# Kernel optimization log

Measured on AMD Instinct MI355X. Metric: run time of the kernel, lower is better.

Reference implementation:

```python
import jax, jax.numpy as jnp
import numpy as np

N = 4096
CIN = 128
COUT = 128
J = 2
SLOPE = 0.2        # LeakyReLU negative slope (GAT-style)
NEG = -9.0e15      # mask fill value from the source
ATT = J * COUT     # att_slice


def _leaky(v):
    return jnp.where(v >= 0, v, SLOPE * v)


def setup_inputs() -> dict:
    key = jax.random.key(0)
    ks = jax.random.split(key, 12)
    x = jax.random.normal(ks[0], (N, CIN), dtype=jnp.float32)

    def sparse_op(k):
        kv, km = jax.random.split(k)
        vals = jax.random.normal(kv, (N, N), dtype=jnp.float32)
        mask = jax.random.uniform(km, (N, N)) < 0.05
        return jnp.where(mask, vals, 0.0)

    Lu = sparse_op(ks[1])
    Ld = sparse_op(ks[2])
    P = jax.random.normal(ks[3], (N, N), dtype=jnp.float32) * 0.01  # harmonic projector

    s = 1.0 / np.sqrt(CIN)
    Wi_w = jax.random.uniform(ks[4], (J, CIN, COUT), minval=-s, maxval=s)
    Wi_b = jax.random.uniform(ks[5], (J, COUT), minval=-s, maxval=s)
    Ws_w = jax.random.uniform(ks[6], (J, CIN, COUT), minval=-s, maxval=s)
    Ws_b = jax.random.uniform(ks[7], (J, COUT), minval=-s, maxval=s)
    Wh_w = jax.random.uniform(ks[8], (CIN, COUT), minval=-s, maxval=s)
    Wh_b = jax.random.uniform(ks[9], (COUT,), minval=-s, maxval=s)
    att_irr = jax.random.normal(ks[10], (2 * ATT, 1), dtype=jnp.float32) * 0.1
    att_sol = jax.random.normal(ks[11], (2 * ATT, 1), dtype=jnp.float32) * 0.1
    return {"x": x, "Lu": Lu, "Ld": Ld, "P": P,
            "Wi_w": Wi_w, "Wi_b": Wi_b, "Ws_w": Ws_w, "Ws_b": Ws_b,
            "Wh_w": Wh_w, "Wh_b": Wh_b, "att_irr": att_irr, "att_sol": att_sol}


def reference(x, Lu, Ld, P, Wi_w, Wi_b, Ws_w, Ws_b, Wh_w, Wh_b, att_irr, att_sol):
    n = x.shape[0]
    # concat_j W_irr[j](x) -> [N, J*COUT] (j-major matches torch.cat along dim=1)
    x_irr = (jnp.einsum('nc,jco->njo', x, Wi_w) + Wi_b[None]).reshape(n, ATT)
    x_sol = (jnp.einsum('nc,jco->njo', x, Ws_w) + Ws_b[None]).reshape(n, ATT)

    # GAT-style scores: E[i,j] = leaky(s1[i] + s2[j])
    E_irr = _leaky(x_irr @ att_irr[:ATT] + (x_irr @ att_irr[ATT:]).T)
    E_sol = _leaky(x_sol @ att_sol[:ATT] + (x_sol @ att_sol[ATT:]).T)
    E_irr = jnp.where(Ld != 0, E_irr, NEG)
    E_sol = jnp.where(Lu != 0, E_sol, NEG)
    alpha_irr = jax.nn.softmax(E_irr, axis=1)  # dropout: eval mode -> identity
    alpha_sol = jax.nn.softmax(E_sol, axis=1)

    z = (alpha_irr @ x) @ Wi_w[0] + Wi_b[0] + (alpha_sol @ x) @ Ws_w[0] + Ws_b[0]
    for p in range(1, J):  # Laplacian-power aggregation
        alpha_irr = alpha_irr @ Ld
        alpha_sol = alpha_sol @ Lu
        z = z + (alpha_irr @ x) @ Wi_w[p] + Wi_b[p]
        z = z + (alpha_sol @ x) @ Ws_w[p] + Ws_b[p]
    z = z + (P @ x) @ Wh_w + Wh_b
    return z
```

## Files before the change

kernel.cpp:

```cpp
#include <hip/hip_runtime.h>

#define NN 4096
#define IDX_CAP 512
#define SEG_CAP 160
#define SLOPE 0.2f

typedef float f4_t __attribute__((ext_vector_type(4)));

#define V_OFF     0
#define C_OFF     512
#define BT_OFF    516
#define S_OFF     1024
#define HXI_OFF   32768
#define HXS_OFF   (HXI_OFF + NN*128)
#define UI_OFF    (HXS_OFF + NN*128)
#define US_OFF    (UI_OFF + NN*128)
#define XWH_OFF   (US_OFF + NN*128)
#define OI_OFF    (XWH_OFF + NN*128)
#define OS_OFF    (OI_OFF + NN*128)
#define ZP_OFF    (OS_OFF + NN*128)
#define WS_FLOATS (ZP_OFF + 8*NN*128)
#define IDX_BYTE_OFF ((size_t)WS_FLOATS * 4)
#define CNT_BYTE_OFF (IDX_BYTE_OFF + (size_t)2*NN*IDX_CAP*2)

#define XI(c)   ((c) + (((c) >> 5) << 2))

#define MAP_BR(bid)   (((bid) >> 2) & 1)
#define MAP_ROW(bid)  ((((bid) >> 3) << 2) | ((bid) & 3))

__global__ __launch_bounds__(128) void k_prep(
    const float* __restrict__ Wi_w, const float* __restrict__ Wi_b,
    const float* __restrict__ Ws_w, const float* __restrict__ Ws_b,
    const float* __restrict__ Wh_b, const float* __restrict__ att_irr,
    const float* __restrict__ att_sol, float* __restrict__ ws) {
  const int t = threadIdx.x;
  float v1i = 0.f, v2i = 0.f, v1s = 0.f, v2s = 0.f;
  for (int j = 0; j < 2; ++j) {
    for (int o = 0; o < 128; ++o) {
      const float wi = Wi_w[j*16384 + t*128 + o];
      const float wv = Ws_w[j*16384 + t*128 + o];
      v1i += wi * att_irr[j*128 + o];
      v2i += wi * att_irr[256 + j*128 + o];
      v1s += wv * att_sol[j*128 + o];
      v2s += wv * att_sol[256 + j*128 + o];
    }
  }
  ws[V_OFF + t]       = v1i;
  ws[V_OFF + 128 + t] = v2i;
  ws[V_OFF + 256 + t] = v1s;
  ws[V_OFF + 384 + t] = v2s;
  ws[BT_OFF + t] = Wi_b[t] + Wi_b[128 + t] + Ws_b[t] + Ws_b[128 + t] + Wh_b[t];
  if (t < 4) {
    const float* bb = (t < 2) ? Wi_b : Ws_b;
    const float* aa = ((t < 2) ? att_irr : att_sol) + ((t & 1) ? 256 : 0);
    float c = 0.f;
    for (int k = 0; k < 256; ++k) c += bb[k] * aa[k];
    ws[C_OFF + t] = c;
  }
}

__global__ __launch_bounds__(256) void k_pre2(
    const float* __restrict__ x, const float* __restrict__ Wh_w,
    float* __restrict__ ws) {
  __shared__ __align__(16) float At[32][33];
  __shared__ __align__(16) float Wt[32][144];
  const int t = threadIdx.x;

  if (blockIdx.x < 128) {
    const int rb = blockIdx.x;
    float* out = ws + XWH_OFF;
    const int rg = t >> 4, cg = t & 15;
    const int r0 = rb * 32;
    float acc[2][8];
    #pragma unroll
    for (int i = 0; i < 2; ++i)
      #pragma unroll
      for (int j = 0; j < 8; ++j) acc[i][j] = 0.f;
    for (int k0 = 0; k0 < 128; k0 += 32) {
      __syncthreads();
      {
        const int row = t >> 3, kq = t & 7;
        const float4 av = *(const float4*)&x[(r0 + row)*128 + k0 + kq*4];
        At[row][kq*4+0] = av.x; At[row][kq*4+1] = av.y;
        At[row][kq*4+2] = av.z; At[row][kq*4+3] = av.w;
      }
      #pragma unroll
      for (int l = 0; l < 4; ++l) {
        const int idx = t + l*256;
        const int kr = idx >> 5, c4 = idx & 31;
        const float4 wv = *(const float4*)&Wh_w[(k0 + kr)*128 + c4*4];
        *(float4*)&Wt[kr][XI(c4*4)] = wv;
      }
      __syncthreads();
      #pragma unroll
      for (int k = 0; k < 32; ++k) {
        const float a0 = At[rg*2 + 0][k];
        const float a1 = At[rg*2 + 1][k];
        const float4 b0 = *(const float4*)&Wt[k][XI(cg*8)];
        const float4 b1 = *(const float4*)&Wt[k][XI(cg*8 + 4)];
        acc[0][0] += a0*b0.x; acc[0][1] += a0*b0.y; acc[0][2] += a0*b0.z; acc[0][3] += a0*b0.w;
        acc[0][4] += a0*b1.x; acc[0][5] += a0*b1.y; acc[0][6] += a0*b1.z; acc[0][7] += a0*b1.w;
        acc[1][0] += a1*b0.x; acc[1][1] += a1*b0.y; acc[1][2] += a1*b0.z; acc[1][3] += a1*b0.w;
        acc[1][4] += a1*b1.x; acc[1][5] += a1*b1.y; acc[1][6] += a1*b1.z; acc[1][7] += a1*b1.w;
      }
    }
    #pragma unroll
    for (int i = 0; i < 2; ++i) {
      const int r = r0 + rg*2 + i;
      #pragma unroll
      for (int j = 0; j < 8; ++j) out[r*128 + cg*8 + j] = acc[i][j];
    }
  } else {
    const int wave = t >> 6, lane = t & 63;
    const int row = (blockIdx.x - 128) * 4 + wave;
    const float* v = ws + V_OFF;
    const float x0 = x[row*128 + lane];
    const float x1 = x[row*128 + 64 + lane];
    float p0 = x0 * v[lane]       + x1 * v[64 + lane];
    float p1 = x0 * v[128 + lane] + x1 * v[192 + lane];
    float p2 = x0 * v[256 + lane] + x1 * v[320 + lane];
    float p3 = x0 * v[384 + lane] + x1 * v[448 + lane];
    #pragma unroll
    for (int off = 32; off; off >>= 1) {
      p0 += __shfl_down(p0, off);
      p1 += __shfl_down(p1, off);
      p2 += __shfl_down(p2, off);
      p3 += __shfl_down(p3, off);
    }
    if (lane == 0) {
      ws[S_OFF + row]          = p0 + ws[C_OFF + 0];
      ws[S_OFF + NN + row]     = p1 + ws[C_OFF + 1];
      ws[S_OFF + 2*NN + row]   = p2 + ws[C_OFF + 2];
      ws[S_OFF + 3*NN + row]   = p3 + ws[C_OFF + 3];
    }
  }
}

__global__ __launch_bounds__(256) void k_spmm_emit(
    const float* __restrict__ Ld, const float* __restrict__ Lu,
    const float* __restrict__ x, float* __restrict__ ws,
    unsigned short* __restrict__ idxbuf, int* __restrict__ cntbuf) {
  const int bid = blockIdx.x;
  const int br  = MAP_BR(bid);
  const int row = MAP_ROW(bid);
  const float* __restrict__ Lrow = (br ? Lu : Ld) + (size_t)row * NN;
  float* __restrict__ Hx = ws + (br ? HXS_OFF : HXI_OFF);
  unsigned short* __restrict__ idxg = idxbuf + (size_t)(br*NN + row) * IDX_CAP;
  const int t = threadIdx.x;
  const int w = t >> 6, lane = t & 63;
  const unsigned long long lmask = (1ull << lane) - 1ull;

  __shared__ short jseg[4][SEG_CAP];
  __shared__ float vseg[4][SEG_CAP];
  __shared__ int   wcnt[4];
  __shared__ int   off[5];
  __shared__ short jl[IDX_CAP];
  __shared__ float vl[IDX_CAP];
  __shared__ float red[4][128];

  const f4_t* __restrict__ Lrow4 = (const f4_t*)Lrow;
  f4_t lv[4];
  #pragma unroll
  for (int i = 0; i < 4; ++i) lv[i] = __builtin_nontemporal_load(&Lrow4[i*256 + t]);

  int base = 0;
  #pragma unroll
  for (int i = 0; i < 4; ++i) {
    #pragma unroll
    for (int c = 0; c < 4; ++c) {
      const float v = lv[i][c];
      const unsigned long long bm = __ballot(v != 0.f);
      if (v != 0.f) {
        const int pos = base + (int)__popcll(bm & lmask);
        if (pos < SEG_CAP) {
          jseg[w][pos] = (short)((i*256 + t)*4 + c);
          vseg[w][pos] = v;
        }
      }
      base += (int)__popcll(bm);
    }
  }
  if (lane == 0) wcnt[w] = base;
  __syncthreads();
  if (t == 0) {
    int o = 0, ov = 0;
    #pragma unroll
    for (int s = 0; s < 4; ++s) { off[s] = o; ov |= (wcnt[s] > SEG_CAP); o += wcnt[s]; }
    off[4] = (ov || o > IDX_CAP) ? (IDX_CAP + 1) : o;
    cntbuf[br*NN + row] = off[4];
  }
  __syncthreads();
  const int m = off[4];

  if (m <= IDX_CAP) {
    const int o = off[w], c = wcnt[w];
    for (int k = lane; k < c; k += 64) {
      const short j = jseg[w][k];
      jl[o + k] = j;
      vl[o + k] = vseg[w][k];
      idxg[o + k] = (unsigned short)j;
    }
  }
  __syncthreads();

  if (m <= IDX_CAP) {
    const f4_t* __restrict__ x4 = (const f4_t*)x;
    const int li = lane & 31, half = lane >> 5;
    f4_t acc = {0.f, 0.f, 0.f, 0.f};
    int p = w;
    for (; 2*(p + 12) + 1 < m; p += 16) {
      const int q0 = 2*p + half, q1 = 2*(p+4) + half,
                q2 = 2*(p+8) + half, q3 = 2*(p+12) + half;
      const int j0 = jl[q0], j1 = jl[q1], j2 = jl[q2], j3 = jl[q3];
      const float v0 = vl[q0], v1 = vl[q1], v2 = vl[q2], v3 = vl[q3];
      const f4_t g0 = x4[j0*32 + li];
      const f4_t g1 = x4[j1*32 + li];
      const f4_t g2 = x4[j2*32 + li];
      const f4_t g3 = x4[j3*32 + li];
      acc += v0*g0; acc += v1*g1; acc += v2*g2; acc += v3*g3;
    }
    for (; 2*p < m; p += 4) {
      const int q = 2*p + half;
      if (q < m) acc += vl[q] * x4[jl[q]*32 + li];
    }
    #pragma unroll
    for (int c = 0; c < 4; ++c) acc[c] += __shfl_xor(acc[c], 32);
    if (half == 0) {
      red[w][li*4+0] = acc[0]; red[w][li*4+1] = acc[1];
      red[w][li*4+2] = acc[2]; red[w][li*4+3] = acc[3];
    }
  } else {
    const float2* __restrict__ x2 = (const float2*)x;
    float acc0 = 0.f, acc1 = 0.f;
    for (int j = w*1024; j < (w+1)*1024; ++j) {
      const float v = Lrow[j];
      if (v != 0.f) {
        const float2 g = x2[j*64 + lane];
        acc0 += v*g.x; acc1 += v*g.y;
      }
    }
    red[w][lane*2]     = acc0;
    red[w][lane*2 + 1] = acc1;
  }
  __syncthreads();
  if (t < 128)
    Hx[row*128 + t] = red[0][t] + red[1][t] + red[2][t] + red[3][t];
}

__global__ __launch_bounds__(256) void k_ugemm(
    const float* __restrict__ x, const float* __restrict__ Wi_w,
    const float* __restrict__ Ws_w, float* __restrict__ ws) {
  const int rb = blockIdx.x;
  const int sel = blockIdx.y;
  const float* A[2]; const float* W[2]; float* out;
  if (sel == 0) { A[0]=x; W[0]=Wi_w; A[1]=ws+HXI_OFF; W[1]=Wi_w+16384; out=ws+UI_OFF; }
  else          { A[0]=x; W[0]=Ws_w; A[1]=ws+HXS_OFF; W[1]=Ws_w+16384; out=ws+US_OFF; }

  __shared__ __align__(16) float At[32][33];
  __shared__ __align__(16) float Wt[32][144];
  const int t = threadIdx.x;
  const int rg = t >> 4, cg = t & 15;
  const int r0 = rb * 32;
  float acc[2][8];
  #pragma unroll
  for (int i = 0; i < 2; ++i)
    #pragma unroll
    for (int j = 0; j < 8; ++j) acc[i][j] = 0.f;

  for (int ps = 0; ps < 2; ++ps) {
    const float* __restrict__ Ap = A[ps];
    const float* __restrict__ Wp = W[ps];
    for (int k0 = 0; k0 < 128; k0 += 32) {
      __syncthreads();
      {
        const int row = t >> 3, kq = t & 7;
        const float4 av = *(const float4*)&Ap[(r0 + row)*128 + k0 + kq*4];
        At[row][kq*4+0] = av.x; At[row][kq*4+1] = av.y;
        At[row][kq*4+2] = av.z; At[row][kq*4+3] = av.w;
      }
      #pragma unroll
      for (int l = 0; l < 4; ++l) {
        const int idx = t + l*256;
        const int kr = idx >> 5, c4 = idx & 31;
        const float4 wv = *(const float4*)&Wp[(k0 + kr)*128 + c4*4];
        *(float4*)&Wt[kr][XI(c4*4)] = wv;
      }
      __syncthreads();
      #pragma unroll
      for (int k = 0; k < 32; ++k) {
        const float a0 = At[rg*2 + 0][k];
        const float a1 = At[rg*2 + 1][k];
        const float4 b0 = *(const float4*)&Wt[k][XI(cg*8)];
        const float4 b1 = *(const float4*)&Wt[k][XI(cg*8 + 4)];
        acc[0][0] += a0*b0.x; acc[0][1] += a0*b0.y; acc[0][2] += a0*b0.z; acc[0][3] += a0*b0.w;
        acc[0][4] += a0*b1.x; acc[0][5] += a0*b1.y; acc[0][6] += a0*b1.z; acc[0][7] += a0*b1.w;
        acc[1][0] += a1*b0.x; acc[1][1] += a1*b0.y; acc[1][2] += a1*b0.z; acc[1][3] += a1*b0.w;
        acc[1][4] += a1*b1.x; acc[1][5] += a1*b1.y; acc[1][6] += a1*b1.z; acc[1][7] += a1*b1.w;
      }
    }
  }
  #pragma unroll
  for (int i = 0; i < 2; ++i) {
    const int r = r0 + rg*2 + i;
    #pragma unroll
    for (int j = 0; j < 8; ++j) out[r*128 + cg*8 + j] = acc[i][j];
  }
}

__global__ __launch_bounds__(256) void k_attn(
    const float* __restrict__ Ld, const float* __restrict__ Lu,
    float* __restrict__ ws, const unsigned short* __restrict__ idxbuf,
    const int* __restrict__ cntbuf) {
  const int bid = blockIdx.x;
  const int br  = MAP_BR(bid);
  const int row = MAP_ROW(bid);
  const float* __restrict__ U = ws + (br ? US_OFF : UI_OFF);
  float* __restrict__ O = ws + (br ? OS_OFF : OI_OFF);
  const float s1 = ws[S_OFF + (br ? 2*NN : 0) + row];
  const float* __restrict__ s2a = ws + S_OFF + (br ? 3*NN : NN);
  const int cnt = cntbuf[br*NN + row];
  const int t = threadIdx.x;
  const int w = t >> 6, lane = t & 63;

  __shared__ int   jl[IDX_CAP];
  __shared__ float el[IDX_CAP];
  __shared__ float red[4][128];
  __shared__ float rsum[256];
  __shared__ float dsh[4];

  if (cnt > 0 && cnt <= IDX_CAP) {
    const unsigned short* __restrict__ idx = idxbuf + (size_t)(br*NN + row) * IDX_CAP;
    float dpart = 0.f;
    for (int p = t; p < cnt; p += 256) {
      const int j = idx[p];
      const float sc = s1 + s2a[j];
      const float e = expf(sc >= 0.f ? sc : SLOPE * sc);
      jl[p] = j; el[p] = e; dpart += e;
    }
    rsum[t] = dpart;
    __syncthreads();
    if (t < 128) rsum[t] += rsum[t + 128];
    __syncthreads();
    if (t < 64) {
      float v = rsum[t] + rsum[t + 64];
      #pragma unroll
      for (int off = 32; off; off >>= 1) v += __shfl_down(v, off);
      if (t == 0) dsh[0] = v;
    }
    __syncthreads();
    const float den = dsh[0];
    const f4_t* __restrict__ U4 = (const f4_t*)U;
    const int li = lane & 31, half = lane >> 5;
    f4_t acc = {0.f, 0.f, 0.f, 0.f};
    int p = w;
    for (; 2*(p + 12) + 1 < cnt; p += 16) {
      const int q0 = 2*p + half, q1 = 2*(p+4) + half,
                q2 = 2*(p+8) + half, q3 = 2*(p+12) + half;
      const int j0 = jl[q0], j1 = jl[q1], j2 = jl[q2], j3 = jl[q3];
      const float e0 = el[q0], e1 = el[q1], e2 = el[q2], e3 = el[q3];
      const f4_t g0 = U4[j0*32 + li];
      const f4_t g1 = U4[j1*32 + li];
      const f4_t g2 = U4[j2*32 + li];
      const f4_t g3 = U4[j3*32 + li];
      acc += e0*g0; acc += e1*g1; acc += e2*g2; acc += e3*g3;
    }
    for (; 2*p < cnt; p += 4) {
      const int q = 2*p + half;
      if (q < cnt) acc += el[q] * U4[jl[q]*32 + li];
    }
    #pragma unroll
    for (int c = 0; c < 4; ++c) acc[c] += __shfl_xor(acc[c], 32);
    if (half == 0) {
      red[w][li*4+0] = acc[0]; red[w][li*4+1] = acc[1];
      red[w][li*4+2] = acc[2]; red[w][li*4+3] = acc[3];
    }
    __syncthreads();
    if (t < 128)
      O[row*128 + t] = (red[0][t] + red[1][t] + red[2][t] + red[3][t]) / den;
  } else if (cnt == 0) {
    const float2* __restrict__ U2 = (const float2*)U;
    float acc0 = 0.f, acc1 = 0.f;
    for (int j = w*1024; j < (w+1)*1024; ++j) {
      const float2 g = U2[j*64 + lane];
      acc0 += g.x; acc1 += g.y;
    }
    red[w][lane*2]     = acc0;
    red[w][lane*2 + 1] = acc1;
    __syncthreads();
    if (t < 128)
      O[row*128 + t] = (red[0][t] + red[1][t] + red[2][t] + red[3][t]) * (1.f / NN);
  } else {
    const float* __restrict__ Lrow = (br ? Lu : Ld) + (size_t)row * NN;
    const float2* __restrict__ U2 = (const float2*)U;
    float acc0 = 0.f, acc1 = 0.f, dp = 0.f;
    for (int j = w*1024; j < (w+1)*1024; ++j) {
      const float v = Lrow[j];
      if (v != 0.f) {
        const float sc = s1 + s2a[j];
        const float e = expf(sc >= 0.f ? sc : SLOPE * sc);
        const float2 g = U2[j*64 + lane];
        acc0 += e*g.x; acc1 += e*g.y;
        dp += e;
      }
    }
    if (lane == 0) dsh[w] = dp;
    red[w][lane*2]     = acc0;
    red[w][lane*2 + 1] = acc1;
    __syncthreads();
    const float den = dsh[0] + dsh[1] + dsh[2] + dsh[3];
    if (t < 128)
      O[row*128 + t] = (red[0][t] + red[1][t] + red[2][t] + red[3][t]) / den;
  }
}

__global__ __launch_bounds__(256) void k_pgemm(const float* __restrict__ P,
                                               const float* __restrict__ ws,
                                               float* __restrict__ zpart) {
  const int rbl = blockIdx.x & 63;
  const int nb  = blockIdx.x >> 6;
  const int kz  = blockIdx.y;
  const float* __restrict__ Xw = ws + XWH_OFF;

  __shared__ __align__(16) float Pt[64][33];
  __shared__ __align__(16) float Xt[32][72];
  const int t = threadIdx.x;
  const int rg = t >> 4, cg = t & 15;
  const int r0 = rbl * 64;
  const int c0 = nb * 64;
  const int kbase = kz * 512;
  float acc[4][4];
  #pragma unroll
  for (int i = 0; i < 4; ++i)
    #pragma unroll
    for (int j = 0; j < 4; ++j) acc[i][j] = 0.f;

  for (int k0 = kbase; k0 < kbase + 512; k0 += 32) {
    __syncthreads();
    #pragma unroll
    for (int l = 0; l < 2; ++l) {
      const int idx = t + l*256;
      const int row = idx >> 3, kq = idx & 7;
      const float4 pv = *(const float4*)&P[(size_t)(r0 + row)*NN + k0 + kq*4];
      Pt[row][kq*4+0] = pv.x; Pt[row][kq*4+1] = pv.y;
      Pt[row][kq*4+2] = pv.z; Pt[row][kq*4+3] = pv.w;
    }
    {
      #pragma unroll
      for (int l = 0; l < 2; ++l) {
        const int idx = t + l*256;
        const int kr = idx >> 4, c4 = idx & 15;
        const float4 xv = *(const float4*)&Xw[(k0 + kr)*128 + c0 + c4*4];
        *(float4*)&Xt[kr][XI(c4*4)] = xv;
      }
    }
    __syncthreads();
    #pragma unroll
    for (int k = 0; k < 32; ++k) {
      const float a0 = Pt[rg*4 + 0][k];
      const float a1 = Pt[rg*4 + 1][k];
      const float a2 = Pt[rg*4 + 2][k];
      const float a3 = Pt[rg*4 + 3][k];
      const float4 b = *(const float4*)&Xt[k][XI(cg*4)];
      acc[0][0] += a0*b.x; acc[0][1] += a0*b.y; acc[0][2] += a0*b.z; acc[0][3] += a0*b.w;
      acc[1][0] += a1*b.x; acc[1][1] += a1*b.y; acc[1][2] += a1*b.z; acc[1][3] += a1*b.w;
      acc[2][0] += a2*b.x; acc[2][1] += a2*b.y; acc[2][2] += a2*b.z; acc[2][3] += a2*b.w;
      acc[3][0] += a3*b.x; acc[3][1] += a3*b.y; acc[3][2] += a3*b.z; acc[3][3] += a3*b.w;
    }
  }
  float* __restrict__ zp = zpart + (size_t)kz * NN * 128;
  #pragma unroll
  for (int i = 0; i < 4; ++i) {
    const int r = r0 + rg*4 + i;
    #pragma unroll
    for (int j = 0; j < 4; ++j) zp[r*128 + c0 + cg*4 + j] = acc[i][j];
  }
}

__global__ __launch_bounds__(256) void k_combine(const float* __restrict__ ws,
                                                 float* __restrict__ z) {
  const int i = blockIdx.x * 256 + threadIdx.x;
  const int col = i & 127;
  float acc = ws[BT_OFF + col] + ws[OI_OFF + i] + ws[OS_OFF + i];
  #pragma unroll
  for (int kz = 0; kz < 8; ++kz) acc += ws[ZP_OFF + kz*NN*128 + i];
  z[i] = acc;
}

extern "C" void kernel_launch(void* const* d_in, const int* in_sizes, int n_in,
                              void* d_out, int out_size, void* d_ws, size_t ws_size,
                              hipStream_t stream) {
  const float* x       = (const float*)d_in[0];
  const float* Lu      = (const float*)d_in[1];
  const float* Ld      = (const float*)d_in[2];
  const float* P       = (const float*)d_in[3];
  const float* Wi_w    = (const float*)d_in[4];
  const float* Wi_b    = (const float*)d_in[5];
  const float* Ws_w    = (const float*)d_in[6];
  const float* Ws_b    = (const float*)d_in[7];
  const float* Wh_w    = (const float*)d_in[8];
  const float* Wh_b    = (const float*)d_in[9];
  const float* att_irr = (const float*)d_in[10];
  const float* att_sol = (const float*)d_in[11];
  float* z  = (float*)d_out;
  float* ws = (float*)d_ws;
  unsigned short* idxbuf = (unsigned short*)((char*)d_ws + IDX_BYTE_OFF);
  int*            cntbuf = (int*)((char*)d_ws + CNT_BYTE_OFF);
  float*          zpart  = ws + ZP_OFF;

  k_prep<<<1, 128, 0, stream>>>(Wi_w, Wi_b, Ws_w, Ws_b, Wh_b, att_irr, att_sol, ws);
  k_pre2<<<1152, 256, 0, stream>>>(x, Wh_w, ws);
  k_spmm_emit<<<2 * NN, 256, 0, stream>>>(Ld, Lu, x, ws, idxbuf, cntbuf);
  {
    dim3 g(128, 2);
    k_ugemm<<<g, 256, 0, stream>>>(x, Wi_w, Ws_w, ws);
  }
  k_attn<<<2 * NN, 256, 0, stream>>>(Ld, Lu, ws, idxbuf, cntbuf);
  {
    dim3 g(128, 8);
    k_pgemm<<<g, 256, 0, stream>>>(P, ws, zpart);
  }
  k_combine<<<NN * 128 / 256, 256, 0, stream>>>(ws, z);
}
```

Measured before the change: 373.5 us.

## Enlarge P-GEMM tiles to 128x128 and deepen gather unrolling in sparse kernels

Each P GEMM block now computes a full 128-row by 128-column tile with an 8x8 per-thread micro-tile and vectorized float4 stores, so P is read once instead of twice across column blocks. The grid shrinks from 128x8 to 32x8 blocks, which trades less global traffic for fewer blocks and higher register use. Separately, the gather loops in the sparse emit and attention kernels get an extra 8-way unrolled stage so more independent x/U row loads are in flight per iteration.

```diff
diff --git a/kernel.cpp b/kernel.cpp
--- a/kernel.cpp
+++ b/kernel.cpp
@@ -208,16 +208,31 @@
     const int li = lane & 31, half = lane >> 5;
     f4_t acc = {0.f, 0.f, 0.f, 0.f};
     int p = w;
+    for (; 2*(p + 28) + 1 < m; p += 32) {
+      int jj[8]; float vv[8];
+      #pragma unroll
+      for (int u = 0; u < 8; ++u) {
+        const int q = 2*(p + 4*u) + half;
+        jj[u] = jl[q]; vv[u] = vl[q];
+      }
+      f4_t gg[8];
+      #pragma unroll
+      for (int u = 0; u < 8; ++u) gg[u] = x4[jj[u]*32 + li];
+      #pragma unroll
+      for (int u = 0; u < 8; ++u) acc += vv[u] * gg[u];
+    }
     for (; 2*(p + 12) + 1 < m; p += 16) {
-      const int q0 = 2*p + half, q1 = 2*(p+4) + half,
-                q2 = 2*(p+8) + half, q3 = 2*(p+12) + half;
-      const int j0 = jl[q0], j1 = jl[q1], j2 = jl[q2], j3 = jl[q3];
-      const float v0 = vl[q0], v1 = vl[q1], v2 = vl[q2], v3 = vl[q3];
-      const f4_t g0 = x4[j0*32 + li];
-      const f4_t g1 = x4[j1*32 + li];
-      const f4_t g2 = x4[j2*32 + li];
-      const f4_t g3 = x4[j3*32 + li];
-      acc += v0*g0; acc += v1*g1; acc += v2*g2; acc += v3*g3;
+      int jj[4]; float vv[4];
+      #pragma unroll
+      for (int u = 0; u < 4; ++u) {
+        const int q = 2*(p + 4*u) + half;
+        jj[u] = jl[q]; vv[u] = vl[q];
+      }
+      f4_t gg[4];
+      #pragma unroll
+      for (int u = 0; u < 4; ++u) gg[u] = x4[jj[u]*32 + li];
+      #pragma unroll
+      for (int u = 0; u < 4; ++u) acc += vv[u] * gg[u];
     }
     for (; 2*p < m; p += 4) {
       const int q = 2*p + half;
@@ -353,16 +368,31 @@
     const int li = lane & 31, half = lane >> 5;
     f4_t acc = {0.f, 0.f, 0.f, 0.f};
     int p = w;
+    for (; 2*(p + 28) + 1 < cnt; p += 32) {
+      int jj[8]; float ee[8];
+      #pragma unroll
+      for (int u = 0; u < 8; ++u) {
+        const int q = 2*(p + 4*u) + half;
+        jj[u] = jl[q]; ee[u] = el[q];
+      }
+      f4_t gg[8];
+      #pragma unroll
+      for (int u = 0; u < 8; ++u) gg[u] = U4[jj[u]*32 + li];
+      #pragma unroll
+      for (int u = 0; u < 8; ++u) acc += ee[u] * gg[u];
+    }
     for (; 2*(p + 12) + 1 < cnt; p += 16) {
-      const int q0 = 2*p + half, q1 = 2*(p+4) + half,
-                q2 = 2*(p+8) + half, q3 = 2*(p+12) + half;
-      const int j0 = jl[q0], j1 = jl[q1], j2 = jl[q2], j3 = jl[q3];
-      const float e0 = el[q0], e1 = el[q1], e2 = el[q2], e3 = el[q3];
-      const f4_t g0 = U4[j0*32 + li];
-      const f4_t g1 = U4[j1*32 + li];
-      const f4_t g2 = U4[j2*32 + li];
-      const f4_t g3 = U4[j3*32 + li];
-      acc += e0*g0; acc += e1*g1; acc += e2*g2; acc += e3*g3;
+      int jj[4]; float ee[4];
+      #pragma unroll
+      for (int u = 0; u < 4; ++u) {
+        const int q = 2*(p + 4*u) + half;
+        jj[u] = jl[q]; ee[u] = el[q];
+      }
+      f4_t gg[4];
+      #pragma unroll
+      for (int u = 0; u < 4; ++u) gg[u] = U4[jj[u]*32 + li];
+      #pragma unroll
+      for (int u = 0; u < 4; ++u) acc += ee[u] * gg[u];
     }
     for (; 2*p < cnt; p += 4) {
       const int q = 2*p + half;
@@ -416,63 +446,65 @@
 __global__ __launch_bounds__(256) void k_pgemm(const float* __restrict__ P,
                                                const float* __restrict__ ws,
                                                float* __restrict__ zpart) {
-  const int rbl = blockIdx.x & 63;
-  const int nb  = blockIdx.x >> 6;
+  const int rbl = blockIdx.x;
   const int kz  = blockIdx.y;
   const float* __restrict__ Xw = ws + XWH_OFF;
 
-  __shared__ __align__(16) float Pt[64][33];
-  __shared__ __align__(16) float Xt[32][72];
+  __shared__ __align__(16) float Pt[128][33];
+  __shared__ __align__(16) float Xt[32][144];
   const int t = threadIdx.x;
   const int rg = t >> 4, cg = t & 15;
-  const int r0 = rbl * 64;
-  const int c0 = nb * 64;
+  const int r0 = rbl * 128;
   const int kbase = kz * 512;
-  float acc[4][4];
-  #pragma unroll
-  for (int i = 0; i < 4; ++i)
-    #pragma unroll
-    for (int j = 0; j < 4; ++j) acc[i][j] = 0.f;
+  float acc[8][8];
+  #pragma unroll
+  for (int i = 0; i < 8; ++i)
+    #pragma unroll
+    for (int j = 0; j < 8; ++j) acc[i][j] = 0.f;
 
   for (int k0 = kbase; k0 < kbase + 512; k0 += 32) {
     __syncthreads();
     #pragma unroll
-    for (int l = 0; l < 2; ++l) {
+    for (int l = 0; l < 4; ++l) {
       const int idx = t + l*256;
       const int row = idx >> 3, kq = idx & 7;
       const float4 pv = *(const float4*)&P[(size_t)(r0 + row)*NN + k0 + kq*4];
       Pt[row][kq*4+0] = pv.x; Pt[row][kq*4+1] = pv.y;
       Pt[row][kq*4+2] = pv.z; Pt[row][kq*4+3] = pv.w;
     }
-    {
-      #pragma unroll
-      for (int l = 0; l < 2; ++l) {
-        const int idx = t + l*256;
-        const int kr = idx >> 4, c4 = idx & 15;
-        const float4 xv = *(const float4*)&Xw[(k0 + kr)*128 + c0 + c4*4];
-        *(float4*)&Xt[kr][XI(c4*4)] = xv;
-      }
+    #pragma unroll
+    for (int l = 0; l < 4; ++l) {
+      const int idx = t + l*256;
+      const int kr = idx >> 5, c4 = idx & 31;
+      const float4 xv = *(const float4*)&Xw[(k0 + kr)*128 + c4*4];
+      *(float4*)&Xt[kr][XI(c4*4)] = xv;
     }
     __syncthreads();
     #pragma unroll
     for (int k = 0; k < 32; ++k) {
-      const float a0 = Pt[rg*4 + 0][k];
-      const float a1 = Pt[rg*4 + 1][k];
-      const float a2 = Pt[rg*4 + 2][k];
-      const float a3 = Pt[rg*4 + 3][k];
-      const float4 b = *(const float4*)&Xt[k][XI(cg*4)];
-      acc[0][0] += a0*b.x; acc[0][1] += a0*b.y; acc[0][2] += a0*b.z; acc[0][3] += a0*b.w;
-      acc[1][0] += a1*b.x; acc[1][1] += a1*b.y; acc[1][2] += a1*b.z; acc[1][3] += a1*b.w;
-      acc[2][0] += a2*b.x; acc[2][1] += a2*b.y; acc[2][2] += a2*b.z; acc[2][3] += a2*b.w;
-      acc[3][0] += a3*b.x; acc[3][1] += a3*b.y; acc[3][2] += a3*b.z; acc[3][3] += a3*b.w;
+      float a[8];
+      #pragma unroll
+      for (int i = 0; i < 8; ++i) a[i] = Pt[rg*8 + i][k];
+      const float4 b0 = *(const float4*)&Xt[k][XI(cg*8)];
+      const float4 b1 = *(const float4*)&Xt[k][XI(cg*8 + 4)];
+      #pragma unroll
+      for (int i = 0; i < 8; ++i) {
+        acc[i][0] += a[i]*b0.x; acc[i][1] += a[i]*b0.y;
+        acc[i][2] += a[i]*b0.z; acc[i][3] += a[i]*b0.w;
+        acc[i][4] += a[i]*b1.x; acc[i][5] += a[i]*b1.y;
+        acc[i][6] += a[i]*b1.z; acc[i][7] += a[i]*b1.w;
+      }
     }
   }
   float* __restrict__ zp = zpart + (size_t)kz * NN * 128;
   #pragma unroll
-  for (int i = 0; i < 4; ++i) {
-    const int r = r0 + rg*4 + i;
-    #pragma unroll
-    for (int j = 0; j < 4; ++j) zp[r*128 + c0 + cg*4 + j] = acc[i][j];
+  for (int i = 0; i < 8; ++i) {
+    const int r = r0 + rg*8 + i;
+    float4 o0, o1;
+    o0.x = acc[i][0]; o0.y = acc[i][1]; o0.z = acc[i][2]; o0.w = acc[i][3];
+    o1.x = acc[i][4]; o1.y = acc[i][5]; o1.z = acc[i][6]; o1.w = acc[i][7];
+    *(float4*)&zp[r*128 + cg*8]     = o0;
+    *(float4*)&zp[r*128 + cg*8 + 4] = o1;
   }
 }
 
@@ -516,7 +548,7 @@
   }
   k_attn<<<2 * NN, 256, 0, stream>>>(Ld, Lu, ws, idxbuf, cntbuf);
   {
-    dim3 g(128, 8);
+    dim3 g(32, 8);
     k_pgemm<<<g, 256, 0, stream>>>(P, ws, zpart);
   }
   k_combine<<<NN * 128 / 256, 256, 0, stream>>>(ws, z);
```

Result: slower. 388.1 us (+3.9%).

## Use split-bf16 MFMA for the dense P @ (x Wh) GEMM

Applied to the files above, without the earlier changes.

The dense P×(xWh) GEMM moves from scalar FP32 LDS-tiled FMA to 32x32x16 bf16 MFMA instructions. Each operand is split into high and low bf16 parts, and three MFMAs per tile keep the result close to FP32 accuracy. k_pre2 now writes xWh transposed as hi/lo bf16 arrays so the B operand can be read directly from global memory. Each block splits K across wave pairs and reduces through LDS. This replaces the FP32 ALU bottleneck with matrix-core work, at the cost of extra conversion work, uncoalesced transposed stores and reading P straight from global without LDS staging.

```diff
diff --git a/kernel.cpp b/kernel.cpp
--- a/kernel.cpp
+++ b/kernel.cpp
@@ -6,6 +6,8 @@
 #define SLOPE 0.2f
 
 typedef float f4_t __attribute__((ext_vector_type(4)));
+typedef __bf16 bf8v __attribute__((ext_vector_type(8)));
+typedef float f32x16 __attribute__((ext_vector_type(16)));
 
 #define V_OFF     0
 #define C_OFF     512
@@ -28,6 +30,15 @@
 #define MAP_BR(bid)   (((bid) >> 2) & 1)
 #define MAP_ROW(bid)  ((((bid) >> 3) << 2) | ((bid) & 3))
 
+__device__ __forceinline__ unsigned short f2bf(float x) {
+  unsigned u = __float_as_uint(x);
+  return (unsigned short)((u + 0x7FFFu + ((u >> 16) & 1u)) >> 16);
+}
+__device__ __forceinline__ float bf2f(unsigned short h) {
+  return __uint_as_float(((unsigned)h) << 16);
+}
+union BFU { unsigned short u[8]; bf8v v; };
+
 __global__ __launch_bounds__(128) void k_prep(
     const float* __restrict__ Wi_w, const float* __restrict__ Wi_b,
     const float* __restrict__ Ws_w, const float* __restrict__ Ws_b,
@@ -61,14 +72,14 @@
 
 __global__ __launch_bounds__(256) void k_pre2(
     const float* __restrict__ x, const float* __restrict__ Wh_w,
-    float* __restrict__ ws) {
+    float* __restrict__ ws, unsigned short* __restrict__ xth,
+    unsigned short* __restrict__ xtl) {
   __shared__ __align__(16) float At[32][33];
   __shared__ __align__(16) float Wt[32][144];
   const int t = threadIdx.x;
 
   if (blockIdx.x < 128) {
     const int rb = blockIdx.x;
-    float* out = ws + XWH_OFF;
     const int rg = t >> 4, cg = t & 15;
     const int r0 = rb * 32;
     float acc[2][8];
@@ -108,7 +119,14 @@
     for (int i = 0; i < 2; ++i) {
       const int r = r0 + rg*2 + i;
       #pragma unroll
-      for (int j = 0; j < 8; ++j) out[r*128 + cg*8 + j] = acc[i][j];
+      for (int j = 0; j < 8; ++j) {
+        const int c = cg*8 + j;
+        const float val = acc[i][j];
+        const unsigned short h = f2bf(val);
+        const unsigned short l = f2bf(val - bf2f(h));
+        xth[(size_t)c*NN + r] = h;
+        xtl[(size_t)c*NN + r] = l;
+      }
     }
   } else {
     const int wave = t >> 6, lane = t & 63;
@@ -413,66 +431,70 @@
   }
 }
 
-__global__ __launch_bounds__(256) void k_pgemm(const float* __restrict__ P,
-                                               const float* __restrict__ ws,
-                                               float* __restrict__ zpart) {
-  const int rbl = blockIdx.x & 63;
-  const int nb  = blockIdx.x >> 6;
-  const int kz  = blockIdx.y;
-  const float* __restrict__ Xw = ws + XWH_OFF;
-
-  __shared__ __align__(16) float Pt[64][33];
-  __shared__ __align__(16) float Xt[32][72];
+__global__ __launch_bounds__(256) void k_pgemm(
+    const float* __restrict__ P, const unsigned short* __restrict__ xth,
+    const unsigned short* __restrict__ xtl, float* __restrict__ zpart) {
   const int t = threadIdx.x;
-  const int rg = t >> 4, cg = t & 15;
-  const int r0 = rbl * 64;
-  const int c0 = nb * 64;
-  const int kbase = kz * 512;
-  float acc[4][4];
+  const int w = t >> 6, lane = t & 63;
+  const int mt = w & 1, kh = w >> 1;
+  const int la = lane & 31;
+  const int koff = (lane >> 5) * 8;
+  const int r0 = blockIdx.x * 64;
+  const int kz = blockIdx.y;
+  const int kb = kz * 512 + kh * 256;
+
+  f32x16 acc[4];
   #pragma unroll
-  for (int i = 0; i < 4; ++i)
-    #pragma unroll
-    for (int j = 0; j < 4; ++j) acc[i][j] = 0.f;
-
-  for (int k0 = kbase; k0 < kbase + 512; k0 += 32) {
-    __syncthreads();
-    #pragma unroll
-    for (int l = 0; l < 2; ++l) {
-      const int idx = t + l*256;
-      const int row = idx >> 3, kq = idx & 7;
-      const float4 pv = *(const float4*)&P[(size_t)(r0 + row)*NN + k0 + kq*4];
-      Pt[row][kq*4+0] = pv.x; Pt[row][kq*4+1] = pv.y;
-      Pt[row][kq*4+2] = pv.z; Pt[row][kq*4+3] = pv.w;
-    }
-    {
-      #pragma unroll
-      for (int l = 0; l < 2; ++l) {
-        const int idx = t + l*256;
-        const int kr = idx >> 4, c4 = idx & 15;
-        const float4 xv = *(const float4*)&Xw[(k0 + kr)*128 + c0 + c4*4];
-        *(float4*)&Xt[kr][XI(c4*4)] = xv;
-      }
-    }
-    __syncthreads();
-    #pragma unroll
-    for (int k = 0; k < 32; ++k) {
-      const float a0 = Pt[rg*4 + 0][k];
-      const float a1 = Pt[rg*4 + 1][k];
-      const float a2 = Pt[rg*4 + 2][k];
-      const float a3 = Pt[rg*4 + 3][k];
-      const float4 b = *(const float4*)&Xt[k][XI(cg*4)];
-      acc[0][0] += a0*b.x; acc[0][1] += a0*b.y; acc[0][2] += a0*b.z; acc[0][3] += a0*b.w;
-      acc[1][0] += a1*b.x; acc[1][1] += a1*b.y; acc[1][2] += a1*b.z; acc[1][3] += a1*b.w;
-      acc[2][0] += a2*b.x; acc[2][1] += a2*b.y; acc[2][2] += a2*b.z; acc[2][3] += a2*b.w;
-      acc[3][0] += a3*b.x; acc[3][1] += a3*b.y; acc[3][2] += a3*b.z; acc[3][3] += a3*b.w;
-    }
-  }
-  float* __restrict__ zp = zpart + (size_t)kz * NN * 128;
-  #pragma unroll
-  for (int i = 0; i < 4; ++i) {
-    const int r = r0 + rg*4 + i;
-    #pragma unroll
-    for (int j = 0; j < 4; ++j) zp[r*128 + c0 + cg*4 + j] = acc[i][j];
+  for (int n = 0; n < 4; ++n)
+    #pragma unroll
+    for (int e = 0; e < 16; ++e) acc[n][e] = 0.f;
+
+  const float* __restrict__ arow = P + (size_t)(r0 + 32*mt + la) * NN + kb + koff;
+
+  for (int s = 0; s < 16; ++s) {
+    const int kk = s * 16;
+    const float4 a0 = *(const float4*)(arow + kk);
+    const float4 a1 = *(const float4*)(arow + kk + 4);
+    BFU ah, al;
+    #pragma unroll
+    for (int i = 0; i < 8; ++i) {
+      const float f = (i < 4) ? (&a0.x)[i] : (&a1.x)[i - 4];
+      const unsigned short h = f2bf(f);
+      ah.u[i] = h;
+      al.u[i] = f2bf(f - bf2f(h));
+    }
+    #pragma unroll
+    for (int n = 0; n < 4; ++n) {
+      const size_t boff = (size_t)(32*n + la) * NN + kb + kk + koff;
+      const bf8v bh = *(const bf8v*)(xth + boff);
+      const bf8v bl = *(const bf8v*)(xtl + boff);
+      acc[n] = __builtin_amdgcn_mfma_f32_32x32x16_bf16(ah.v, bh, acc[n], 0, 0, 0);
+      acc[n] = __builtin_amdgcn_mfma_f32_32x32x16_bf16(al.v, bh, acc[n], 0, 0, 0);
+      acc[n] = __builtin_amdgcn_mfma_f32_32x32x16_bf16(ah.v, bl, acc[n], 0, 0, 0);
+    }
+  }
+
+  __shared__ float red[2][32][128];
+  if (kh == 0) {
+    #pragma unroll
+    for (int n = 0; n < 4; ++n)
+      #pragma unroll
+      for (int reg = 0; reg < 16; ++reg) {
+        const int row = (reg & 3) + 8*(reg >> 2) + 4*(lane >> 5);
+        red[mt][row][32*n + la] = acc[n][reg];
+      }
+  }
+  __syncthreads();
+  if (kh == 1) {
+    float* __restrict__ zp = zpart + (size_t)kz * NN * 128;
+    #pragma unroll
+    for (int n = 0; n < 4; ++n)
+      #pragma unroll
+      for (int reg = 0; reg < 16; ++reg) {
+        const int row = (reg & 3) + 8*(reg >> 2) + 4*(lane >> 5);
+        zp[(size_t)(r0 + 32*mt + row) * 128 + 32*n + la] =
+            red[mt][row][32*n + la] + acc[n][reg];
+      }
   }
 }
 
@@ -506,9 +528,11 @@
   unsigned short* idxbuf = (unsigned short*)((char*)d_ws + IDX_BYTE_OFF);
   int*            cntbuf = (int*)((char*)d_ws + CNT_BYTE_OFF);
   float*          zpart  = ws + ZP_OFF;
+  unsigned short* xth    = (unsigned short*)(ws + XWH_OFF);
+  unsigned short* xtl    = xth + (size_t)128 * NN;
 
   k_prep<<<1, 128, 0, stream>>>(Wi_w, Wi_b, Ws_w, Ws_b, Wh_b, att_irr, att_sol, ws);
-  k_pre2<<<1152, 256, 0, stream>>>(x, Wh_w, ws);
+  k_pre2<<<1152, 256, 0, stream>>>(x, Wh_w, ws, xth, xtl);
   k_spmm_emit<<<2 * NN, 256, 0, stream>>>(Ld, Lu, x, ws, idxbuf, cntbuf);
   {
     dim3 g(128, 2);
@@ -516,8 +540,8 @@
   }
   k_attn<<<2 * NN, 256, 0, stream>>>(Ld, Lu, ws, idxbuf, cntbuf);
   {
-    dim3 g(128, 8);
-    k_pgemm<<<g, 256, 0, stream>>>(P, ws, zpart);
+    dim3 g(64, 8);
+    k_pgemm<<<g, 256, 0, stream>>>(P, xth, xtl, zpart);
   }
   k_combine<<<NN * 128 / 256, 256, 0, stream>>>(ws, z);
 }
```

New measurement: 362.5 us. -2.9%, faster.
